# Kernel optimization log

Measured on AMD Instinct MI355X. Metric: run time of the kernel, lower is better.

The kernel has to match this reference:

```python
import jax, jax.numpy as jnp
import numpy as np

N, F, E, T = 50000, 128, 800000, 8


def setup_inputs() -> dict:
    key = jax.random.key(0)
    ks = jax.random.split(key, 10)
    s = 1.0 / np.sqrt(F)
    return {
        "x": jax.random.normal(ks[0], (N, F), jnp.float32),
        "edge_index": jax.random.randint(ks[1], (2, E), 0, N, jnp.int64),
        "edge_weight": jax.random.uniform(ks[2], (E,), jnp.float32),
        "W0": jax.random.normal(ks[3], (F, F), jnp.float32) * s,
        "Wih": jax.random.normal(ks[4], (3 * F, F), jnp.float32) * s,
        "Whh": jax.random.normal(ks[5], (3 * F, F), jnp.float32) * s,
        "bih": jax.random.normal(ks[6], (3 * F,), jnp.float32) * s,
        "bhh": jax.random.normal(ks[7], (3 * F,), jnp.float32) * s,
        "Wlin": jax.random.normal(ks[8], (T, F), jnp.float32) * s,
        "blin": jax.random.normal(ks[9], (T,), jnp.float32) * s,
    }


def _evolve_weight(W0, Wih, Whh, bih, bhh):
    # One GRU step with input = hidden = W0 (rows of weight matrix as batch).
    gi = W0 @ Wih.T + bih  # [F, 3F]
    gh = W0 @ Whh.T + bhh
    ir, iz, inn = jnp.split(gi, 3, axis=1)
    hr, hz, hn = jnp.split(gh, 3, axis=1)
    r = jax.nn.sigmoid(ir + hr)
    z = jax.nn.sigmoid(iz + hz)
    n = jnp.tanh(inn + r * hn)
    return (1.0 - z) * n + z * W0  # [F, F]


def reference(x, edge_index, edge_weight, W0, Wih, Whh, bih, bhh, Wlin, blin):
    n_nodes = x.shape[0]
    W = _evolve_weight(W0, Wih, Whh, bih, bhh)
    # gcn_norm with added self-loops (fill value 1.0), symmetric normalization
    loop = jnp.arange(n_nodes, dtype=edge_index.dtype)
    row = jnp.concatenate([edge_index[0], loop])
    col = jnp.concatenate([edge_index[1], loop])
    ew = jnp.concatenate([edge_weight, jnp.ones((n_nodes,), edge_weight.dtype)])
    deg = jax.ops.segment_sum(ew, col, num_segments=n_nodes)
    dinv = jnp.where(deg > 0, jax.lax.rsqrt(jnp.where(deg > 0, deg, 1.0)), 0.0)
    norm = dinv[row] * ew * dinv[col]  # [E+N]
    xw = x @ W  # [N, F]
    h = jax.ops.segment_sum(norm[:, None] * xw[row], col, num_segments=n_nodes)
    h = jax.nn.relu(h)
    return h @ Wlin.T + blin  # [N, n_target]
```

## Files before the change

### kernel.cpp

```cpp
#include <hip/hip_runtime.h>
#include <math.h>

#define F 128
#define FIX_SCALE 16777216.0f
#define FIX_INV   (1.0f / 16777216.0f)
#define CNT_SHIFT 40
#define DEG_MASK  ((1ULL << 40) - 1)
#define EVB 256

using bf16x8 = __attribute__((ext_vector_type(8))) short;
using f32x4  = __attribute__((ext_vector_type(4))) float;

__device__ inline int read_idx(const int* ei, long long elem, int i64) {
    return i64 ? (int)((const long long*)ei)[elem] : ei[elem];
}
__device__ inline unsigned int f2bf_rn(float f) {
    unsigned int b = __float_as_uint(f);
    return (b + 0x7FFFu + ((b >> 16) & 1u)) >> 16;
}
__device__ inline float bflo(unsigned int u) { return __uint_as_float(u << 16); }
__device__ inline float bfhi(unsigned int u) { return __uint_as_float(u & 0xFFFF0000u); }

__device__ inline void acc8(float* acc, float wt, uint4 v) {
    acc[0] += wt * bflo(v.x); acc[1] += wt * bfhi(v.x);
    acc[2] += wt * bflo(v.y); acc[3] += wt * bfhi(v.y);
    acc[4] += wt * bflo(v.z); acc[5] += wt * bfhi(v.z);
    acc[6] += wt * bflo(v.w); acc[7] += wt * bfhi(v.w);
}

__device__ inline int detect_i64(const int* ei, int* sh) {
    if (threadIdx.x == 0) {
        int i64 = 1;
        for (int j = 0; j < 32; ++j) if (ei[2 * j + 1] != 0) { i64 = 0; break; }
        *sh = i64;
    }
    __syncthreads();
    return *sh;
}

__global__ __launch_bounds__(256) void k_count_evolve(
        const int* __restrict__ ei, const float* __restrict__ ew,
        unsigned long long* __restrict__ packed8, int* __restrict__ pos,
        int E, int N,
        const float* __restrict__ W0, const float* __restrict__ Wih,
        const float* __restrict__ Whh, const float* __restrict__ bih,
        const float* __restrict__ bhh,
        unsigned short* __restrict__ Wth, unsigned short* __restrict__ Wtl) {
    __shared__ int i64sh;
    int wave = threadIdx.x >> 6, lane = threadIdx.x & 63;
    if ((int)blockIdx.x >= EVB) {
        int i64 = detect_i64(ei, &i64sh);
        int e = ((int)blockIdx.x - EVB) * 256 + threadIdx.x;
        if (e >= E) return;
        int c = read_idx(ei, (long long)E + e, i64);
        int copy = blockIdx.x & 7;
        unsigned long long u = (1ULL << CNT_SHIFT) |
                               (unsigned long long)(ew[e] * FIX_SCALE + 0.5f);
        unsigned long long old = atomicAdd(&packed8[(size_t)copy * N + c], u);
        pos[e] = (int)(((unsigned int)(old >> CNT_SHIFT)) | ((unsigned int)copy << 24));
        return;
    }
    int gw = (int)blockIdx.x * 4 + wave;
    int pairBase = gw * 16;
    int i = pairBase >> 7;
    int jb = pairBase & 127;
    int lp = lane & 15, sl = lane >> 4;
    int j = jb + lp;
    const float* w0p = W0 + (size_t)i * F;
    const float* pir = Wih + (size_t)j * F;
    const float* piz = Wih + (size_t)(j + F) * F;
    const float* pin = Wih + (size_t)(j + 2 * F) * F;
    const float* phr = Whh + (size_t)j * F;
    const float* phz = Whh + (size_t)(j + F) * F;
    const float* phn = Whh + (size_t)(j + 2 * F) * F;
    float air = 0, aiz = 0, ain = 0, ahr = 0, ahz = 0, ahn = 0;
    int k0 = sl * 32;
    #pragma unroll
    for (int kk = 0; kk < 32; kk += 4) {
        int k = k0 + kk;
        float4 w0 = *(const float4*)&w0p[k];
        float4 a;
        a = *(const float4*)&pir[k]; air += w0.x*a.x + w0.y*a.y + w0.z*a.z + w0.w*a.w;
        a = *(const float4*)&piz[k]; aiz += w0.x*a.x + w0.y*a.y + w0.z*a.z + w0.w*a.w;
        a = *(const float4*)&pin[k]; ain += w0.x*a.x + w0.y*a.y + w0.z*a.z + w0.w*a.w;
        a = *(const float4*)&phr[k]; ahr += w0.x*a.x + w0.y*a.y + w0.z*a.z + w0.w*a.w;
        a = *(const float4*)&phz[k]; ahz += w0.x*a.x + w0.y*a.y + w0.z*a.z + w0.w*a.w;
        a = *(const float4*)&phn[k]; ahn += w0.x*a.x + w0.y*a.y + w0.z*a.z + w0.w*a.w;
    }
    air += __shfl_xor(air, 16, 64); air += __shfl_xor(air, 32, 64);
    aiz += __shfl_xor(aiz, 16, 64); aiz += __shfl_xor(aiz, 32, 64);
    ain += __shfl_xor(ain, 16, 64); ain += __shfl_xor(ain, 32, 64);
    ahr += __shfl_xor(ahr, 16, 64); ahr += __shfl_xor(ahr, 32, 64);
    ahz += __shfl_xor(ahz, 16, 64); ahz += __shfl_xor(ahz, 32, 64);
    ahn += __shfl_xor(ahn, 16, 64); ahn += __shfl_xor(ahn, 32, 64);
    if (sl == 0) {
        air += bih[j];          ahr += bhh[j];
        aiz += bih[j + F];      ahz += bhh[j + F];
        ain += bih[j + 2 * F];  ahn += bhh[j + 2 * F];
        float r = 1.0f / (1.0f + expf(-(air + ahr)));
        float z = 1.0f / (1.0f + expf(-(aiz + ahz)));
        float n = tanhf(ain + r * ahn);
        float w = (1.0f - z) * n + z * w0p[j];
        unsigned int hb = f2bf_rn(w);
        float whi = __uint_as_float(hb << 16);
        unsigned int lb = f2bf_rn(w - whi);
        Wth[j * F + i] = (unsigned short)hb;
        Wtl[j * F + i] = (unsigned short)lb;
    }
}

__global__ void k_bsum(const unsigned long long* __restrict__ packed8,
                       int* __restrict__ bsum, int N) {
    __shared__ int s[4];
    int i = blockIdx.x * 256 + threadIdx.x;
    int v = 0;
    if (i < N) {
        #pragma unroll
        for (int k = 0; k < 8; ++k)
            v += (int)(packed8[(size_t)k * N + i] >> CNT_SHIFT);
    }
    #pragma unroll
    for (int o = 1; o < 64; o <<= 1) v += __shfl_xor(v, o, 64);
    if ((threadIdx.x & 63) == 0) s[threadIdx.x >> 6] = v;
    __syncthreads();
    if (threadIdx.x == 0) bsum[blockIdx.x] = s[0] + s[1] + s[2] + s[3];
}

__global__ void k_offs(const unsigned long long* __restrict__ packed8,
                       const int* __restrict__ bsum,
                       int* __restrict__ off, int* __restrict__ copyBase,
                       float* __restrict__ dinv, int N, int E, int nblk) {
    __shared__ int sdata[256];
    __shared__ int sred[4];
    __shared__ int sbase;
    int t = threadIdx.x;
    int b = blockIdx.x;
    int base = 0;
    for (int s0 = 0; s0 < nblk; s0 += 256) {
        int idx = s0 + t;
        int v = (idx < nblk && idx < b) ? bsum[idx] : 0;
        #pragma unroll
        for (int o = 1; o < 64; o <<= 1) v += __shfl_xor(v, o, 64);
        if ((t & 63) == 0) sred[t >> 6] = v;
        __syncthreads();
        if (t == 0) sbase = sred[0] + sred[1] + sred[2] + sred[3];
        __syncthreads();
        base += sbase;
        __syncthreads();
    }
    int i = b * 256 + t;
    int v = 0;
    unsigned long long dsum = 0;
    if (i < N) {
        int run = 0;
        int cb[8];
        #pragma unroll
        for (int k = 0; k < 8; ++k) {
            unsigned long long p = packed8[(size_t)k * N + i];
            cb[k] = run;
            run += (int)(p >> CNT_SHIFT);
            dsum += (p & DEG_MASK);
        }
        v = run;
        #pragma unroll
        for (int k = 0; k < 8; ++k) copyBase[(size_t)i * 8 + k] = cb[k];
    }
    sdata[t] = v;
    __syncthreads();
    #pragma unroll
    for (int s = 1; s < 256; s <<= 1) {
        int add = (t >= s) ? sdata[t - s] : 0;
        __syncthreads();
        sdata[t] += add;
        __syncthreads();
    }
    if (i < N) {
        off[i] = base + sdata[t] - v;
        dinv[i] = rsqrtf(1.0f + (float)dsum * FIX_INV);
        if (i == N - 1) off[N] = E;
    }
}

__global__ __launch_bounds__(256) void k_place_cast(
        const int* __restrict__ ei, const float* __restrict__ ew,
        const int* __restrict__ off, const int* __restrict__ copyBase,
        const int* __restrict__ pos,
        int2* __restrict__ ep, int E, int placeBlocks,
        const float2* __restrict__ x2, const float* __restrict__ dinv,
        unsigned int* __restrict__ xs, int M) {
    __shared__ int i64sh;
    if ((int)blockIdx.x < placeBlocks) {
        int i64 = detect_i64(ei, &i64sh);
        int e = blockIdx.x * 256 + threadIdx.x;
        if (e >= E) return;
        int r = read_idx(ei, e, i64);
        int c = read_idx(ei, (long long)E + e, i64);
        int pe = pos[e];
        int slot = off[c] + copyBase[(size_t)c * 8 + ((unsigned int)pe >> 24)] + (pe & 0xFFFFFF);
        ep[slot] = make_int2(r, __float_as_int(ew[e]));
    } else {
        int id = ((int)blockIdx.x - placeBlocks) * 256 + threadIdx.x;
        if (id >= M) return;
        float di = dinv[id >> 6];
        float2 v = x2[id];
        xs[id] = f2bf_rn(di * v.x) | (f2bf_rn(di * v.y) << 16);
    }
}

__global__ __launch_bounds__(256) void k_agg2(const uint4* __restrict__ xs4,
                                              const int* __restrict__ off,
                                              const int2* __restrict__ ep,
                                              const float* __restrict__ dinv,
                                              uint4* __restrict__ hagg4, int N) {
    int wave = threadIdx.x >> 6, lane = threadIdx.x & 63;
    int c = blockIdx.x * 4 + wave;
    if (c >= N) return;
    int g = lane >> 4, sl = lane & 15;
    int start = off[c], end = off[c + 1];
    float di = dinv[c];
    float a0[8] = {0,0,0,0,0,0,0,0}, a1[8] = {0,0,0,0,0,0,0,0};
    if (g == 0) {
        uint4 v = xs4[(size_t)c * 16 + sl];
        a0[0] = bflo(v.x); a0[1] = bfhi(v.x);
        a0[2] = bflo(v.y); a0[3] = bfhi(v.y);
        a0[4] = bflo(v.z); a0[5] = bfhi(v.z);
        a0[6] = bflo(v.w); a0[7] = bfhi(v.w);
    }
    int last = end - 1;
    for (int k = start; k < end; k += 16) {
        int iA = k + g, iB = k + g + 4, iC = k + g + 8, iD = k + g + 12;
        int2 eA = ep[min(iA, last)];
        int2 eB = ep[min(iB, last)];
        int2 eC = ep[min(iC, last)];
        int2 eD = ep[min(iD, last)];
        uint4 vA = xs4[(size_t)eA.x * 16 + sl];
        uint4 vB = xs4[(size_t)eB.x * 16 + sl];
        uint4 vC = xs4[(size_t)eC.x * 16 + sl];
        uint4 vD = xs4[(size_t)eD.x * 16 + sl];
        float wA = (iA <= last) ? __int_as_float(eA.y) : 0.f;
        float wB = (iB <= last) ? __int_as_float(eB.y) : 0.f;
        float wC = (iC <= last) ? __int_as_float(eC.y) : 0.f;
        float wD = (iD <= last) ? __int_as_float(eD.y) : 0.f;
        acc8(a0, wA, vA);
        acc8(a1, wB, vB);
        acc8(a0, wC, vC);
        acc8(a1, wD, vD);
    }
    #pragma unroll
    for (int f = 0; f < 8; ++f) {
        float v = a0[f] + a1[f];
        v += __shfl_xor(v, 16, 64);
        v += __shfl_xor(v, 32, 64);
        a0[f] = v;
    }
    if (lane < 16) {
        uint4 o;
        o.x = f2bf_rn(di * a0[0]) | (f2bf_rn(di * a0[1]) << 16);
        o.y = f2bf_rn(di * a0[2]) | (f2bf_rn(di * a0[3]) << 16);
        o.z = f2bf_rn(di * a0[4]) | (f2bf_rn(di * a0[5]) << 16);
        o.w = f2bf_rn(di * a0[6]) | (f2bf_rn(di * a0[7]) << 16);
        hagg4[(size_t)c * 16 + lane] = o;
    }
}

__global__ __launch_bounds__(256) void k_gemm(const uint4* __restrict__ hagg4,
                                              const unsigned short* __restrict__ Wth,
                                              const unsigned short* __restrict__ Wtl,
                                              const float* __restrict__ Wlin,
                                              const float* __restrict__ blin,
                                              float* __restrict__ out, int N) {
    __shared__ __align__(16) unsigned int At[64 * 68];
    __shared__ __align__(16) float WlinL[8 * F];
    int t = threadIdx.x;
    int row0 = blockIdx.x * 64;
    #pragma unroll
    for (int it = 0; it < 4; ++it) {
        int idx = it * 256 + t;
        int rr = idx >> 4, c4 = idx & 15;
        uint4 v = make_uint4(0u, 0u, 0u, 0u);
        if (row0 + rr < N) v = hagg4[(size_t)(row0 + rr) * 16 + c4];
        *(uint4*)&At[rr * 68 + c4 * 4] = v;
    }
    *(float4*)&WlinL[t * 4] = *(const float4*)&Wlin[t * 4];
    __syncthreads();

    int wave = t >> 6, lane = t & 63;
    int sl = lane & 15, q = lane >> 4;
    const unsigned short* Ash = (const unsigned short*)At;
    int mrow = wave * 16 + sl;

    f32x4 acc[8];
    #pragma unroll
    for (int nt = 0; nt < 8; ++nt) acc[nt] = (f32x4){0.f, 0.f, 0.f, 0.f};
    #pragma unroll
    for (int ko = 0; ko < 4; ++ko) {
        bf16x8 a = *(const bf16x8*)&Ash[mrow * 136 + ko * 32 + q * 8];
        #pragma unroll
        for (int nt = 0; nt < 8; ++nt) {
            int boff = (nt * 16 + sl) * F + ko * 32 + q * 8;
            bf16x8 bh = *(const bf16x8*)&Wth[boff];
            bf16x8 bl = *(const bf16x8*)&Wtl[boff];
            acc[nt] = __builtin_amdgcn_mfma_f32_16x16x32_bf16(a, bh, acc[nt], 0, 0, 0);
            acc[nt] = __builtin_amdgcn_mfma_f32_16x16x32_bf16(a, bl, acc[nt], 0, 0, 0);
        }
    }
    #pragma unroll
    for (int nt = 0; nt < 8; ++nt)
        #pragma unroll
        for (int r = 0; r < 4; ++r) acc[nt][r] = fmaxf(acc[nt][r], 0.f);

    float p[8][4];
    #pragma unroll
    for (int tt = 0; tt < 8; ++tt) {
        float wl[8];
        #pragma unroll
        for (int nt = 0; nt < 8; ++nt) wl[nt] = WlinL[tt * F + nt * 16 + sl];
        #pragma unroll
        for (int r = 0; r < 4; ++r) {
            float s = 0.f;
            #pragma unroll
            for (int nt = 0; nt < 8; ++nt) s += acc[nt][r] * wl[nt];
            p[tt][r] = s;
        }
    }
    #pragma unroll
    for (int tt = 0; tt < 8; ++tt)
        #pragma unroll
        for (int r = 0; r < 4; ++r) {
            float v = p[tt][r];
            v += __shfl_xor(v, 1, 64); v += __shfl_xor(v, 2, 64);
            v += __shfl_xor(v, 4, 64); v += __shfl_xor(v, 8, 64);
            p[tt][r] = v;
        }
    if (sl == 0) {
        #pragma unroll
        for (int r = 0; r < 4; ++r) {
            int row = row0 + wave * 16 + q * 4 + r;
            if (row < N) {
                #pragma unroll
                for (int tt = 0; tt < 8; ++tt)
                    out[(size_t)row * 8 + tt] = p[tt][r] + blin[tt];
            }
        }
    }
}

extern "C" void kernel_launch(void* const* d_in, const int* in_sizes, int n_in,
                              void* d_out, int out_size, void* d_ws, size_t ws_size,
                              hipStream_t stream) {
    const float* x    = (const float*)d_in[0];
    const int*   ei   = (const int*)d_in[1];
    const float* ew   = (const float*)d_in[2];
    const float* W0   = (const float*)d_in[3];
    const float* Wih  = (const float*)d_in[4];
    const float* Whh  = (const float*)d_in[5];
    const float* bih  = (const float*)d_in[6];
    const float* bhh  = (const float*)d_in[7];
    const float* Wlin = (const float*)d_in[8];
    const float* blin = (const float*)d_in[9];
    int N = in_sizes[0] / F;
    int E = in_sizes[1] / 2;
    float* outp = (float*)d_out;

    int nblk = (N + 255) / 256;
    int cntBlocks = (E + 255) / 256;
    int M = N * 64;
    int M8 = N * 8;

    char* wsb = (char*)d_ws;
    size_t cur = 0;
    auto alloc = [&](size_t sz) -> void* {
        void* p = wsb + cur;
        cur = (cur + sz + 255) & ~(size_t)255;
        return p;
    };
    unsigned long long* packed8 = (unsigned long long*)alloc((size_t)M8 * 8);
    float* dinv = (float*)alloc((size_t)N * 4);
    int*   off  = (int*)  alloc((size_t)(N + 1) * 4);
    int*   bsum = (int*)  alloc((size_t)nblk * 4);
    int*   pos  = (int*)  alloc((size_t)E * 4);
    int*   copyBase = (int*)alloc((size_t)N * 8 * 4);
    int2*  ep   = (int2*) alloc((size_t)E * 8);
    unsigned short* Wth = (unsigned short*)alloc((size_t)F * F * 2);
    unsigned short* Wtl = (unsigned short*)alloc((size_t)F * F * 2);
    unsigned int* xs    = (unsigned int*)alloc((size_t)N * 64 * 4);
    unsigned int* hagg  = (unsigned int*)alloc((size_t)N * 64 * 4);
    (void)ws_size; (void)n_in; (void)out_size;

    hipMemsetAsync(packed8, 0, (size_t)M8 * 8, stream);
    hipLaunchKernelGGL(k_count_evolve, dim3(EVB + cntBlocks), dim3(256), 0, stream,
                       ei, ew, packed8, pos, E, N,
                       W0, Wih, Whh, bih, bhh, Wth, Wtl);
    hipLaunchKernelGGL(k_bsum, dim3(nblk), dim3(256), 0, stream, packed8, bsum, N);
    hipLaunchKernelGGL(k_offs, dim3(nblk), dim3(256), 0, stream,
                       packed8, bsum, off, copyBase, dinv, N, E, nblk);
    hipLaunchKernelGGL(k_place_cast, dim3(cntBlocks + (M + 255) / 256), dim3(256), 0, stream,
                       ei, ew, off, copyBase, pos, ep, E, cntBlocks,
                       (const float2*)x, dinv, xs, M);
    hipLaunchKernelGGL(k_agg2, dim3((N + 3) / 4), dim3(256), 0, stream,
                       (const uint4*)xs, off, ep, dinv, (uint4*)hagg, N);
    hipLaunchKernelGGL(k_gemm, dim3((N + 63) / 64), dim3(256), 0, stream,
                       (const uint4*)hagg, Wth, Wtl, Wlin, blin, outp, N);
}
```

Before: 217.8 us.

## Fuse aggregation into GEMM via shared memory and shrink degree counters to 32-bit

Merges the neighbour-aggregation kernel and the MFMA GEMM into one 1024-thread block per 64 rows. The aggregated bf16 rows go straight into shared memory instead of being written to and reread from a global buffer, and one launch is removed. Separately, the packed count/degree atomics change from 64-bit to 32-bit words (8-bit count, 18-bit fixed-point weight) and copyBase shrinks to bytes, cutting atomic and scan traffic. The narrower fields risk overflow if a node receives 256 or more edges in one copy, and they coarsen degree precision. Only 4 of the 16 waves do the GEMM, and larger blocks may reduce occupancy.

```diff
diff --git a/kernel.cpp b/kernel.cpp
--- a/kernel.cpp
+++ b/kernel.cpp
@@ -2,10 +2,8 @@
 #include <math.h>
 
 #define F 128
-#define FIX_SCALE 16777216.0f
-#define FIX_INV   (1.0f / 16777216.0f)
-#define CNT_SHIFT 40
-#define DEG_MASK  ((1ULL << 40) - 1)
+#define FIX18     262144.0f
+#define INV18     (1.0f / 262144.0f)
 #define EVB 256
 
 using bf16x8 = __attribute__((ext_vector_type(8))) short;
@@ -40,7 +38,7 @@
 
 __global__ __launch_bounds__(256) void k_count_evolve(
         const int* __restrict__ ei, const float* __restrict__ ew,
-        unsigned long long* __restrict__ packed8, int* __restrict__ pos,
+        unsigned int* __restrict__ packed8, int* __restrict__ pos,
         int E, int N,
         const float* __restrict__ W0, const float* __restrict__ Wih,
         const float* __restrict__ Whh, const float* __restrict__ bih,
@@ -53,11 +51,10 @@
         int e = ((int)blockIdx.x - EVB) * 256 + threadIdx.x;
         if (e >= E) return;
         int c = read_idx(ei, (long long)E + e, i64);
-        int copy = blockIdx.x & 7;
-        unsigned long long u = (1ULL << CNT_SHIFT) |
-                               (unsigned long long)(ew[e] * FIX_SCALE + 0.5f);
-        unsigned long long old = atomicAdd(&packed8[(size_t)copy * N + c], u);
-        pos[e] = (int)(((unsigned int)(old >> CNT_SHIFT)) | ((unsigned int)copy << 24));
+        unsigned int copy = blockIdx.x & 7;
+        unsigned int u = (1u << 24) | (unsigned int)(ew[e] * FIX18 + 0.5f);
+        unsigned int old = atomicAdd(&packed8[(size_t)copy * N + c], u);
+        pos[e] = (int)((old >> 24) | (copy << 24));
         return;
     }
     int gw = (int)blockIdx.x * 4 + wave;
@@ -109,7 +106,7 @@
     }
 }
 
-__global__ void k_bsum(const unsigned long long* __restrict__ packed8,
+__global__ void k_bsum(const unsigned int* __restrict__ packed8,
                        int* __restrict__ bsum, int N) {
     __shared__ int s[4];
     int i = blockIdx.x * 256 + threadIdx.x;
@@ -117,7 +114,7 @@
     if (i < N) {
         #pragma unroll
         for (int k = 0; k < 8; ++k)
-            v += (int)(packed8[(size_t)k * N + i] >> CNT_SHIFT);
+            v += (int)(packed8[(size_t)k * N + i] >> 24);
     }
     #pragma unroll
     for (int o = 1; o < 64; o <<= 1) v += __shfl_xor(v, o, 64);
@@ -126,9 +123,9 @@
     if (threadIdx.x == 0) bsum[blockIdx.x] = s[0] + s[1] + s[2] + s[3];
 }
 
-__global__ void k_offs(const unsigned long long* __restrict__ packed8,
+__global__ void k_offs(const unsigned int* __restrict__ packed8,
                        const int* __restrict__ bsum,
-                       int* __restrict__ off, int* __restrict__ copyBase,
+                       int* __restrict__ off, unsigned char* __restrict__ copyBase,
                        float* __restrict__ dinv, int N, int E, int nblk) {
     __shared__ int sdata[256];
     __shared__ int sred[4];
@@ -150,20 +147,17 @@
     }
     int i = b * 256 + t;
     int v = 0;
-    unsigned long long dsum = 0;
+    unsigned int dsum = 0;
     if (i < N) {
         int run = 0;
-        int cb[8];
         #pragma unroll
         for (int k = 0; k < 8; ++k) {
-            unsigned long long p = packed8[(size_t)k * N + i];
-            cb[k] = run;
-            run += (int)(p >> CNT_SHIFT);
-            dsum += (p & DEG_MASK);
+            unsigned int p = packed8[(size_t)k * N + i];
+            copyBase[(size_t)i * 8 + k] = (unsigned char)run;
+            run += (int)(p >> 24);
+            dsum += (p & 0xFFFFFFu);
         }
         v = run;
-        #pragma unroll
-        for (int k = 0; k < 8; ++k) copyBase[(size_t)i * 8 + k] = cb[k];
     }
     sdata[t] = v;
     __syncthreads();
@@ -176,14 +170,14 @@
     }
     if (i < N) {
         off[i] = base + sdata[t] - v;
-        dinv[i] = rsqrtf(1.0f + (float)dsum * FIX_INV);
+        dinv[i] = rsqrtf(1.0f + (float)dsum * INV18);
         if (i == N - 1) off[N] = E;
     }
 }
 
 __global__ __launch_bounds__(256) void k_place_cast(
         const int* __restrict__ ei, const float* __restrict__ ew,
-        const int* __restrict__ off, const int* __restrict__ copyBase,
+        const int* __restrict__ off, const unsigned char* __restrict__ copyBase,
         const int* __restrict__ pos,
         int2* __restrict__ ep, int E, int placeBlocks,
         const float2* __restrict__ x2, const float* __restrict__ dinv,
@@ -195,8 +189,8 @@
         if (e >= E) return;
         int r = read_idx(ei, e, i64);
         int c = read_idx(ei, (long long)E + e, i64);
-        int pe = pos[e];
-        int slot = off[c] + copyBase[(size_t)c * 8 + ((unsigned int)pe >> 24)] + (pe & 0xFFFFFF);
+        unsigned int pe = (unsigned int)pos[e];
+        int slot = off[c] + (int)copyBase[(size_t)c * 8 + (pe >> 24)] + (int)(pe & 0xFFFFFFu);
         ep[slot] = make_int2(r, __float_as_int(ew[e]));
     } else {
         int id = ((int)blockIdx.x - placeBlocks) * 256 + threadIdx.x;
@@ -207,88 +201,80 @@
     }
 }
 
-__global__ __launch_bounds__(256) void k_agg2(const uint4* __restrict__ xs4,
-                                              const int* __restrict__ off,
-                                              const int2* __restrict__ ep,
-                                              const float* __restrict__ dinv,
-                                              uint4* __restrict__ hagg4, int N) {
-    int wave = threadIdx.x >> 6, lane = threadIdx.x & 63;
-    int c = blockIdx.x * 4 + wave;
-    if (c >= N) return;
-    int g = lane >> 4, sl = lane & 15;
-    int start = off[c], end = off[c + 1];
-    float di = dinv[c];
-    float a0[8] = {0,0,0,0,0,0,0,0}, a1[8] = {0,0,0,0,0,0,0,0};
-    if (g == 0) {
-        uint4 v = xs4[(size_t)c * 16 + sl];
-        a0[0] = bflo(v.x); a0[1] = bfhi(v.x);
-        a0[2] = bflo(v.y); a0[3] = bfhi(v.y);
-        a0[4] = bflo(v.z); a0[5] = bfhi(v.z);
-        a0[6] = bflo(v.w); a0[7] = bfhi(v.w);
-    }
-    int last = end - 1;
-    for (int k = start; k < end; k += 16) {
-        int iA = k + g, iB = k + g + 4, iC = k + g + 8, iD = k + g + 12;
-        int2 eA = ep[min(iA, last)];
-        int2 eB = ep[min(iB, last)];
-        int2 eC = ep[min(iC, last)];
-        int2 eD = ep[min(iD, last)];
-        uint4 vA = xs4[(size_t)eA.x * 16 + sl];
-        uint4 vB = xs4[(size_t)eB.x * 16 + sl];
-        uint4 vC = xs4[(size_t)eC.x * 16 + sl];
-        uint4 vD = xs4[(size_t)eD.x * 16 + sl];
-        float wA = (iA <= last) ? __int_as_float(eA.y) : 0.f;
-        float wB = (iB <= last) ? __int_as_float(eB.y) : 0.f;
-        float wC = (iC <= last) ? __int_as_float(eC.y) : 0.f;
-        float wD = (iD <= last) ? __int_as_float(eD.y) : 0.f;
-        acc8(a0, wA, vA);
-        acc8(a1, wB, vB);
-        acc8(a0, wC, vC);
-        acc8(a1, wD, vD);
-    }
-    #pragma unroll
-    for (int f = 0; f < 8; ++f) {
-        float v = a0[f] + a1[f];
-        v += __shfl_xor(v, 16, 64);
-        v += __shfl_xor(v, 32, 64);
-        a0[f] = v;
-    }
-    if (lane < 16) {
-        uint4 o;
-        o.x = f2bf_rn(di * a0[0]) | (f2bf_rn(di * a0[1]) << 16);
-        o.y = f2bf_rn(di * a0[2]) | (f2bf_rn(di * a0[3]) << 16);
-        o.z = f2bf_rn(di * a0[4]) | (f2bf_rn(di * a0[5]) << 16);
-        o.w = f2bf_rn(di * a0[6]) | (f2bf_rn(di * a0[7]) << 16);
-        hagg4[(size_t)c * 16 + lane] = o;
-    }
-}
-
-__global__ __launch_bounds__(256) void k_gemm(const uint4* __restrict__ hagg4,
-                                              const unsigned short* __restrict__ Wth,
-                                              const unsigned short* __restrict__ Wtl,
-                                              const float* __restrict__ Wlin,
-                                              const float* __restrict__ blin,
-                                              float* __restrict__ out, int N) {
+__global__ __launch_bounds__(1024) void k_agg_gemm(
+        const uint4* __restrict__ xs4, const int* __restrict__ off,
+        const int2* __restrict__ ep, const float* __restrict__ dinv,
+        const unsigned short* __restrict__ Wth, const unsigned short* __restrict__ Wtl,
+        const float* __restrict__ Wlin, const float* __restrict__ blin,
+        float* __restrict__ out, int N) {
     __shared__ __align__(16) unsigned int At[64 * 68];
     __shared__ __align__(16) float WlinL[8 * F];
     int t = threadIdx.x;
+    int wave = t >> 6, lane = t & 63;
     int row0 = blockIdx.x * 64;
-    #pragma unroll
-    for (int it = 0; it < 4; ++it) {
-        int idx = it * 256 + t;
-        int rr = idx >> 4, c4 = idx & 15;
-        uint4 v = make_uint4(0u, 0u, 0u, 0u);
-        if (row0 + rr < N) v = hagg4[(size_t)(row0 + rr) * 16 + c4];
-        *(uint4*)&At[rr * 68 + c4 * 4] = v;
-    }
-    *(float4*)&WlinL[t * 4] = *(const float4*)&Wlin[t * 4];
+    WlinL[t] = Wlin[t];
+    int g = lane >> 4, sl = lane & 15;
+
+    #pragma unroll
+    for (int sub = 0; sub < 4; ++sub) {
+        int rr = wave * 4 + sub;
+        int c = row0 + rr;
+        if (c < N) {
+            int start = off[c], end = off[c + 1];
+            float di = dinv[c];
+            float a0[8] = {0,0,0,0,0,0,0,0}, a1[8] = {0,0,0,0,0,0,0,0};
+            if (g == 0) {
+                uint4 v = xs4[(size_t)c * 16 + sl];
+                a0[0] = bflo(v.x); a0[1] = bfhi(v.x);
+                a0[2] = bflo(v.y); a0[3] = bfhi(v.y);
+                a0[4] = bflo(v.z); a0[5] = bfhi(v.z);
+                a0[6] = bflo(v.w); a0[7] = bfhi(v.w);
+            }
+            int last = end - 1;
+            for (int k = start; k < end; k += 16) {
+                int iA = k + g, iB = k + g + 4, iC = k + g + 8, iD = k + g + 12;
+                int2 eA = ep[min(iA, last)];
+                int2 eB = ep[min(iB, last)];
+                int2 eC = ep[min(iC, last)];
+                int2 eD = ep[min(iD, last)];
+                uint4 vA = xs4[(size_t)eA.x * 16 + sl];
+                uint4 vB = xs4[(size_t)eB.x * 16 + sl];
+                uint4 vC = xs4[(size_t)eC.x * 16 + sl];
+                uint4 vD = xs4[(size_t)eD.x * 16 + sl];
+                float wA = (iA <= last) ? __int_as_float(eA.y) : 0.f;
+                float wB = (iB <= last) ? __int_as_float(eB.y) : 0.f;
+                float wC = (iC <= last) ? __int_as_float(eC.y) : 0.f;
+                float wD = (iD <= last) ? __int_as_float(eD.y) : 0.f;
+                acc8(a0, wA, vA);
+                acc8(a1, wB, vB);
+                acc8(a0, wC, vC);
+                acc8(a1, wD, vD);
+            }
+            #pragma unroll
+            for (int f = 0; f < 8; ++f) {
+                float v = a0[f] + a1[f];
+                v += __shfl_xor(v, 16, 64);
+                v += __shfl_xor(v, 32, 64);
+                a0[f] = v;
+            }
+            if (lane < 16) {
+                uint4 o;
+                o.x = f2bf_rn(di * a0[0]) | (f2bf_rn(di * a0[1]) << 16);
+                o.y = f2bf_rn(di * a0[2]) | (f2bf_rn(di * a0[3]) << 16);
+                o.z = f2bf_rn(di * a0[4]) | (f2bf_rn(di * a0[5]) << 16);
+                o.w = f2bf_rn(di * a0[6]) | (f2bf_rn(di * a0[7]) << 16);
+                *(uint4*)&At[rr * 68 + sl * 4] = o;
+            }
+        } else if (lane < 16) {
+            *(uint4*)&At[rr * 68 + sl * 4] = make_uint4(0u, 0u, 0u, 0u);
+        }
+    }
     __syncthreads();
-
-    int wave = t >> 6, lane = t & 63;
-    int sl = lane & 15, q = lane >> 4;
+    if (wave >= 4) return;
+
+    int q = g;
     const unsigned short* Ash = (const unsigned short*)At;
     int mrow = wave * 16 + sl;
-
     f32x4 acc[8];
     #pragma unroll
     for (int nt = 0; nt < 8; ++nt) acc[nt] = (f32x4){0.f, 0.f, 0.f, 0.f};
@@ -365,7 +351,6 @@
     int nblk = (N + 255) / 256;
     int cntBlocks = (E + 255) / 256;
     int M = N * 64;
-    int M8 = N * 8;
 
     char* wsb = (char*)d_ws;
     size_t cur = 0;
@@ -374,20 +359,19 @@
         cur = (cur + sz + 255) & ~(size_t)255;
         return p;
     };
-    unsigned long long* packed8 = (unsigned long long*)alloc((size_t)M8 * 8);
+    unsigned int* packed8 = (unsigned int*)alloc((size_t)N * 8 * 4);
     float* dinv = (float*)alloc((size_t)N * 4);
     int*   off  = (int*)  alloc((size_t)(N + 1) * 4);
     int*   bsum = (int*)  alloc((size_t)nblk * 4);
     int*   pos  = (int*)  alloc((size_t)E * 4);
-    int*   copyBase = (int*)alloc((size_t)N * 8 * 4);
+    unsigned char* copyBase = (unsigned char*)alloc((size_t)N * 8);
     int2*  ep   = (int2*) alloc((size_t)E * 8);
     unsigned short* Wth = (unsigned short*)alloc((size_t)F * F * 2);
     unsigned short* Wtl = (unsigned short*)alloc((size_t)F * F * 2);
     unsigned int* xs    = (unsigned int*)alloc((size_t)N * 64 * 4);
-    unsigned int* hagg  = (unsigned int*)alloc((size_t)N * 64 * 4);
     (void)ws_size; (void)n_in; (void)out_size;
 
-    hipMemsetAsync(packed8, 0, (size_t)M8 * 8, stream);
+    hipMemsetAsync(packed8, 0, (size_t)N * 8 * 4, stream);
     hipLaunchKernelGGL(k_count_evolve, dim3(EVB + cntBlocks), dim3(256), 0, stream,
                        ei, ew, packed8, pos, E, N,
                        W0, Wih, Whh, bih, bhh, Wth, Wtl);
@@ -397,8 +381,6 @@
     hipLaunchKernelGGL(k_place_cast, dim3(cntBlocks + (M + 255) / 256), dim3(256), 0, stream,
                        ei, ew, off, copyBase, pos, ep, E, cntBlocks,
                        (const float2*)x, dinv, xs, M);
-    hipLaunchKernelGGL(k_agg2, dim3((N + 3) / 4), dim3(256), 0, stream,
-                       (const uint4*)xs, off, ep, dinv, (uint4*)hagg, N);
-    hipLaunchKernelGGL(k_gemm, dim3((N + 63) / 64), dim3(256), 0, stream,
-                       (const uint4*)hagg, Wth, Wtl, Wlin, blin, outp, N);
-}
+    hipLaunchKernelGGL(k_agg_gemm, dim3((N + 63) / 64), dim3(1024), 0, stream,
+                       (const uint4*)xs, off, ep, dinv, Wth, Wtl, Wlin, blin, outp, N);
+}
```

Result: no change. 216.7 us (-0.5%).
